# Kernel optimization log

Hardware: AMD Instinct MI355X
Metric: run time of the kernel (lower is better)

Reference implementation:

```python
import jax, jax.numpy as jnp
import numpy as np

N_NODES = 64
N_EDGES = N_NODES * (N_NODES - 1)  # 4032 (fully connected, no self-loops)
BATCH = 64
N_IN = 64
N_HID = 128
N_OUT = 16


def _linear_params(key, fan_in, fan_out):
    # mimic torch nn.Linear default init: U(-1/sqrt(fan_in), 1/sqrt(fan_in))
    kw, kb = jax.random.split(key)
    s = 1.0 / np.sqrt(fan_in)
    W = jax.random.uniform(kw, (fan_in, fan_out), minval=-s, maxval=s, dtype=jnp.float32)
    b = jax.random.uniform(kb, (fan_out,), minval=-s, maxval=s, dtype=jnp.float32)
    return W, b


def setup_inputs() -> dict:
    key = jax.random.key(0)
    ks = jax.random.split(key, 10)
    # one-hot relation matrices for fully-connected graph without self loops
    pairs = np.array([(i, j) for i in range(N_NODES) for j in range(N_NODES) if i != j])
    eye = np.eye(N_NODES, dtype=np.float32)
    rel_send = jnp.asarray(eye[pairs[:, 0]])  # [E, N]
    rel_rec = jnp.asarray(eye[pairs[:, 1]])   # [E, N]

    x = jax.random.normal(ks[0], (BATCH, N_NODES, N_IN), dtype=jnp.float32)

    w1a, b1a = _linear_params(ks[1], N_IN, N_HID)
    w1b, b1b = _linear_params(ks[2], N_HID, N_HID)
    w2a, b2a = _linear_params(ks[3], 2 * N_HID, N_HID)
    w2b, b2b = _linear_params(ks[4], N_HID, N_HID)
    w3a, b3a = _linear_params(ks[5], N_HID, N_HID)
    w3b, b3b = _linear_params(ks[6], N_HID, N_HID)
    w4a, b4a = _linear_params(ks[7], 3 * N_HID, N_HID)  # factor=True
    w4b, b4b = _linear_params(ks[8], N_HID, N_HID)
    wout, bout = _linear_params(ks[9], N_HID, N_OUT)

    return dict(x=x, rel_rec=rel_rec, rel_send=rel_send,
                w1a=w1a, b1a=b1a, w1b=w1b, b1b=b1b,
                w2a=w2a, b2a=b2a, w2b=w2b, b2b=b2b,
                w3a=w3a, b3a=b3a, w3b=w3b, b3b=b3b,
                w4a=w4a, b4a=b4a, w4b=w4b, b4b=b4b,
                wout=wout, bout=bout)


def _mlp(x, wa, ba, wb, bb):
    # Linear -> ReLU -> Linear
    return jax.nn.relu(x @ wa + ba) @ wb + bb


def reference(x, rel_rec, rel_send,
              w1a, b1a, w1b, b1b,
              w2a, b2a, w2b, b2b,
              w3a, b3a, w3b, b3b,
              w4a, b4a, w4b, b4b,
              wout, bout):
    def node2edge(h):
        receivers = jnp.einsum('en,bnh->beh', rel_rec, h)
        senders = jnp.einsum('en,bnh->beh', rel_send, h)
        return jnp.concatenate([senders, receivers], axis=-1)  # [B,E,2H]

    def edge2node(e):
        agg = jnp.einsum('en,beh->bnh', rel_rec, e)
        norm = rel_rec.sum(0)[None, :, None]  # [1,N,1]
        return agg / (norm + 1e-6)

    h = _mlp(x, w1a, b1a, w1b, b1b)            # [B,N,H]
    e = _mlp(node2edge(h), w2a, b2a, w2b, b2b)  # [B,E,H]
    x_skip = e
    # factor=True branch
    n = _mlp(edge2node(e), w3a, b3a, w3b, b3b)  # [B,N,H]
    e2 = node2edge(n)                           # [B,E,2H]
    e2 = jnp.concatenate([e2, x_skip], axis=2)  # [B,E,3H]
    e2 = _mlp(e2, w4a, b4a, w4b, b4b)           # [B,E,H]
    return e2 @ wout + bout                     # [B,E,n_out]
```

## Files before the change

### kernel.cpp

```cpp
#include <hip/hip_runtime.h>
#include <hip/hip_bf16.h>


#define DI __device__ __forceinline__

typedef short bf16x8 __attribute__((ext_vector_type(8)));
typedef float f32x4 __attribute__((ext_vector_type(4)));
typedef unsigned short u16;

static constexpr int NN = 64, NE = 4032, H = 128;

DI u16 f2bf(float f) {
  union { float f; unsigned u; } v; v.f = f;
  unsigned u = v.u;
  return (u16)((u + 0x7fffu + ((u >> 16) & 1u)) >> 16);
}
DI unsigned pk2(float a, float b) {
  union { __hip_bfloat162 h; unsigned u; } c;
  c.h = __float22bfloat162_rn(float2{a, b});
  return c.u;
}
DI f32x4 mf(bf16x8 a, bf16x8 b, f32x4 c) {
  return __builtin_amdgcn_mfma_f32_16x16x32_bf16(a, b, c, 0, 0, 0);
}
DI bf16x8 ldfrag(const u16* __restrict__ p, int idx, int l) {
  return *reinterpret_cast<const bf16x8*>(p + (idx * 64 + l) * 8);
}
#define PIN_REGS() asm volatile("" ::: "memory")

__global__ __launch_bounds__(64) void prepack_kernel(
    const float* __restrict__ w1a, const float* __restrict__ w1b,
    const float* __restrict__ w2a, const float* __restrict__ w2b,
    const float* __restrict__ w3a, const float* __restrict__ w3b,
    const float* __restrict__ w4a, const float* __restrict__ w4b,
    const float* __restrict__ wout,
    const float* __restrict__ b2b, const float* __restrict__ b4b,
    const float* __restrict__ bout,
    u16* __restrict__ pk, float* __restrict__ c2, float* __restrict__ c4) {
  int seg = blockIdx.y, f = blockIdx.x, l = threadIdx.x;
  int h = l >> 4, mm = l & 15;
  if (seg == 10) {
    if (f >= 4) return;
    union { u16 u[8]; uint4 q; } o;
#pragma unroll
    for (int jj = 0; jj < 8; jj++) {
      int row = f * 32 + (jj >> 2) * 16 + h * 4 + (jj & 3);
      float s = 0.f;
      for (int j = 0; j < 128; j++) s += w4b[row * 128 + j] * wout[j * 16 + mm];
      o.u[jj] = f2bf(s);
    }
    *reinterpret_cast<uint4*>(pk + ((304 + f) * 64 + l) * 8) = o.q;
    return;
  }
  if (seg == 11) {
    if (f < 2) {
      int o = f * 64 + l;
      float s = 0.f;
      for (int k = 0; k < 128; k++) s += b2b[k] * w4a[(256 + k) * 128 + o];
      c2[o] = s;
    } else if (f == 2 && l < 16) {
      float s = bout[l];
      for (int k = 0; k < 128; k++) s += b4b[k] * wout[k * 16 + l];
      c4[l] = s;
    }
    return;
  }
  const float* src; int foff, nfrag, roff, pi;
  switch (seg) {
    case 0:  src = w1a; foff = 0;   nfrag = 16; roff = 0;   pi = 0; break;
    case 1:  src = w1b; foff = 16;  nfrag = 32; roff = 0;   pi = 1; break;
    case 2:  src = w2a; foff = 48;  nfrag = 32; roff = 0;   pi = 1; break;
    case 3:  src = w2a; foff = 80;  nfrag = 32; roff = 128; pi = 1; break;
    case 4:  src = w2b; foff = 112; nfrag = 32; roff = 0;   pi = 0; break;
    case 5:  src = w3a; foff = 144; nfrag = 32; roff = 0;   pi = 1; break;
    case 6:  src = w3b; foff = 176; nfrag = 32; roff = 0;   pi = 1; break;
    case 7:  src = w4a; foff = 208; nfrag = 32; roff = 0;   pi = 1; break;
    case 8:  src = w4a; foff = 240; nfrag = 32; roff = 128; pi = 1; break;
    default: src = w4a; foff = 272; nfrag = 32; roff = 256; pi = 1; break;
  }
  if (f >= nfrag) return;
  int kt = f >> 3, ct = f & 7;
  union { u16 u[8]; uint4 q; } o;
#pragma unroll
  for (int jj = 0; jj < 8; jj++) {
    int row = pi ? (kt * 32 + (jj >> 2) * 16 + h * 4 + (jj & 3))
                 : (kt * 32 + h * 8 + jj);
    o.u[jj] = f2bf(src[(roff + row) * 128 + ct * 16 + mm]);
  }
  *reinterpret_cast<uint4*>(pk + ((foff + f) * 64 + l) * 8) = o.q;
}

__global__ __launch_bounds__(64, 1) void node_kernel(
    const float* __restrict__ x, const u16* __restrict__ pk,
    const float* __restrict__ b1a, const float* __restrict__ b1b,
    const float* __restrict__ b2a,
    float* __restrict__ sproj, float* __restrict__ rproj) {
  int blk = blockIdx.x, b = blk >> 2, nq = blk & 3;
  int l = threadIdx.x, m = l & 15, h = l >> 4;
  int node = nq * 16 + m;
  const f32x4 Z = {0.f, 0.f, 0.f, 0.f};
  bf16x8 wA[32], wB[32];
#pragma unroll
  for (int i = 0; i < 16; i++) wA[i] = ldfrag(pk, i, l);
#pragma unroll
  for (int i = 0; i < 32; i++) wB[i] = ldfrag(pk + 16 * 512, i, l);
  PIN_REGS();
  f32x4 acc[8]; bf16x8 ef[4];
  const float* xb = x + (b * NN + node) * 64;
#pragma unroll
  for (int kt = 0; kt < 2; kt++) {
    f32x4 a0 = *(const f32x4*)(xb + kt * 32 + h * 8);
    f32x4 a1 = *(const f32x4*)(xb + kt * 32 + h * 8 + 4);
    union { unsigned u[4]; bf16x8 v; } t;
    t.u[0] = pk2(a0[0], a0[1]); t.u[1] = pk2(a0[2], a0[3]);
    t.u[2] = pk2(a1[0], a1[1]); t.u[3] = pk2(a1[2], a1[3]);
#pragma unroll
    for (int ft = 0; ft < 8; ft++)
      acc[ft] = mf(wA[kt * 8 + ft], t.v, kt == 0 ? Z : acc[ft]);
  }
#pragma unroll
  for (int k2 = 0; k2 < 4; k2++) {
    f32x4 bA = *(const f32x4*)(b1a + (2 * k2) * 16 + h * 4);
    f32x4 bB = *(const f32x4*)(b1a + (2 * k2 + 1) * 16 + h * 4);
    f32x4 a0 = acc[2 * k2], a1 = acc[2 * k2 + 1];
    union { unsigned u[4]; bf16x8 v; } t;
    t.u[0] = pk2(fmaxf(a0[0] + bA[0], 0.f), fmaxf(a0[1] + bA[1], 0.f));
    t.u[1] = pk2(fmaxf(a0[2] + bA[2], 0.f), fmaxf(a0[3] + bA[3], 0.f));
    t.u[2] = pk2(fmaxf(a1[0] + bB[0], 0.f), fmaxf(a1[1] + bB[1], 0.f));
    t.u[3] = pk2(fmaxf(a1[2] + bB[2], 0.f), fmaxf(a1[3] + bB[3], 0.f));
    ef[k2] = t.v;
  }
#pragma unroll
  for (int i = 0; i < 32; i++) wA[i] = ldfrag(pk + 48 * 512, i, l);
  PIN_REGS();
#pragma unroll
  for (int kt = 0; kt < 4; kt++)
#pragma unroll
    for (int ft = 0; ft < 8; ft++)
      acc[ft] = mf(wB[kt * 8 + ft], ef[kt], kt == 0 ? Z : acc[ft]);
  bf16x8 efh[4];
#pragma unroll
  for (int k2 = 0; k2 < 4; k2++) {
    f32x4 bA = *(const f32x4*)(b1b + (2 * k2) * 16 + h * 4);
    f32x4 bB = *(const f32x4*)(b1b + (2 * k2 + 1) * 16 + h * 4);
    f32x4 a0 = acc[2 * k2], a1 = acc[2 * k2 + 1];
    union { unsigned u[4]; bf16x8 v; } t;
    t.u[0] = pk2(a0[0] + bA[0], a0[1] + bA[1]);
    t.u[1] = pk2(a0[2] + bA[2], a0[3] + bA[3]);
    t.u[2] = pk2(a1[0] + bB[0], a1[1] + bB[1]);
    t.u[3] = pk2(a1[2] + bB[2], a1[3] + bB[3]);
    efh[k2] = t.v;
  }
#pragma unroll
  for (int i = 0; i < 32; i++) wB[i] = ldfrag(pk + 80 * 512, i, l);
  PIN_REGS();
#pragma unroll
  for (int kt = 0; kt < 4; kt++)
#pragma unroll
    for (int ft = 0; ft < 8; ft++)
      acc[ft] = mf(wA[kt * 8 + ft], efh[kt], kt == 0 ? Z : acc[ft]);
  float* spo = sproj + (b * NN + node) * H;
#pragma unroll
  for (int ft = 0; ft < 8; ft++)
    *reinterpret_cast<f32x4*>(spo + ft * 16 + h * 4) = acc[ft];
#pragma unroll
  for (int kt = 0; kt < 4; kt++)
#pragma unroll
    for (int ft = 0; ft < 8; ft++)
      acc[ft] = mf(wB[kt * 8 + ft], efh[kt], kt == 0 ? Z : acc[ft]);
  float* rpo = rproj + (b * NN + node) * H;
#pragma unroll
  for (int ft = 0; ft < 8; ft++) {
    f32x4 bb = *(const f32x4*)(b2a + ft * 16 + h * 4);
    f32x4 o = acc[ft];
    o[0] += bb[0]; o[1] += bb[1]; o[2] += bb[2]; o[3] += bb[3];
    *reinterpret_cast<f32x4*>(rpo + ft * 16 + h * 4) = o;
  }
}

__global__ __launch_bounds__(256, 1) void agg_kernel(
    const float* __restrict__ sproj, const float* __restrict__ rproj,
    const u16* __restrict__ pk,
    const float* __restrict__ b2b, const float* __restrict__ b3a,
    const float* __restrict__ b3b, const float* __restrict__ b4a,
    const float* __restrict__ c2,
    float* __restrict__ s4, float* __restrict__ r4) {
  __shared__ float lred[3][32][65];
  int blk = blockIdx.x, b = blk >> 2, jq = blk & 3;
  int tid = threadIdx.x, l = tid & 63, w = tid >> 6, m = l & 15, h = l >> 4;
  int j = jq * 16 + m;
  const float* rpb = rproj + (b * NN + j) * H;
  f32x4 rpv[8], accS[8];
#pragma unroll
  for (int k = 0; k < 8; k++) {
    rpv[k] = *(const f32x4*)(rpb + (k >> 1) * 32 + h * 8 + (k & 1) * 4);
    accS[k] = f32x4{0.f, 0.f, 0.f, 0.f};
  }
  const float* spb = sproj + b * NN * H;
  for (int i = w * 16; i < w * 16 + 16; i++) {
    const float* sp = spb + i * H;
#pragma unroll
    for (int k = 0; k < 8; k++) {
      f32x4 s = *(const f32x4*)(sp + (k >> 1) * 32 + h * 8 + (k & 1) * 4);
      f32x4 t = s + rpv[k];
      t[0] = fmaxf(t[0], 0.f); t[1] = fmaxf(t[1], 0.f);
      t[2] = fmaxf(t[2], 0.f); t[3] = fmaxf(t[3], 0.f);
      accS[k] += t;
    }
  }
  if (w == jq) {
    const float* sp = spb + j * H;
#pragma unroll
    for (int k = 0; k < 8; k++) {
      f32x4 s = *(const f32x4*)(sp + (k >> 1) * 32 + h * 8 + (k & 1) * 4);
      f32x4 t = s + rpv[k];
      accS[k][0] -= fmaxf(t[0], 0.f); accS[k][1] -= fmaxf(t[1], 0.f);
      accS[k][2] -= fmaxf(t[2], 0.f); accS[k][3] -= fmaxf(t[3], 0.f);
    }
  }
  if (w > 0) {
#pragma unroll
    for (int k = 0; k < 8; k++)
#pragma unroll
      for (int qq = 0; qq < 4; qq++) lred[w - 1][k * 4 + qq][l] = accS[k][qq];
  }
  __syncthreads();
  if (w != 0) return;
#pragma unroll
  for (int ww = 0; ww < 3; ww++)
#pragma unroll
    for (int k = 0; k < 8; k++)
#pragma unroll
      for (int qq = 0; qq < 4; qq++) accS[k][qq] += lred[ww][k * 4 + qq][l];

  const f32x4 Z = {0.f, 0.f, 0.f, 0.f};
  bf16x8 tb[4];
#pragma unroll
  for (int k2 = 0; k2 < 4; k2++) {
    f32x4 a0 = accS[2 * k2], a1 = accS[2 * k2 + 1];
    union { unsigned u[4]; bf16x8 v; } t;
    t.u[0] = pk2(a0[0], a0[1]); t.u[1] = pk2(a0[2], a0[3]);
    t.u[2] = pk2(a1[0], a1[1]); t.u[3] = pk2(a1[2], a1[3]);
    tb[k2] = t.v;
  }
  bf16x8 wA[32], wB[32]; f32x4 acc[8]; bf16x8 ef[4], efn[4];
#pragma unroll
  for (int i = 0; i < 32; i++) wA[i] = ldfrag(pk + 112 * 512, i, l);
#pragma unroll
  for (int i = 0; i < 32; i++) wB[i] = ldfrag(pk + 144 * 512, i, l);
  PIN_REGS();
#pragma unroll
  for (int kt = 0; kt < 4; kt++)
#pragma unroll
    for (int ft = 0; ft < 8; ft++)
      acc[ft] = mf(wA[kt * 8 + ft], tb[kt], kt == 0 ? Z : acc[ft]);
  const float inv = 1.0f / (63.0f + 1e-6f);
  const float binv = 63.0f * inv;
#pragma unroll
  for (int k2 = 0; k2 < 4; k2++) {
    f32x4 bA = *(const f32x4*)(b2b + (2 * k2) * 16 + h * 4);
    f32x4 bB = *(const f32x4*)(b2b + (2 * k2 + 1) * 16 + h * 4);
    f32x4 a0 = acc[2 * k2], a1 = acc[2 * k2 + 1];
    union { unsigned u[4]; bf16x8 v; } t;
    t.u[0] = pk2(a0[0] * inv + bA[0] * binv, a0[1] * inv + bA[1] * binv);
    t.u[1] = pk2(a0[2] * inv + bA[2] * binv, a0[3] * inv + bA[3] * binv);
    t.u[2] = pk2(a1[0] * inv + bB[0] * binv, a1[1] * inv + bB[1] * binv);
    t.u[3] = pk2(a1[2] * inv + bB[2] * binv, a1[3] * inv + bB[3] * binv);
    ef[k2] = t.v;
  }
#pragma unroll
  for (int i = 0; i < 32; i++) wA[i] = ldfrag(pk + 176 * 512, i, l);
  PIN_REGS();
#pragma unroll
  for (int kt = 0; kt < 4; kt++)
#pragma unroll
    for (int ft = 0; ft < 8; ft++)
      acc[ft] = mf(wB[kt * 8 + ft], ef[kt], kt == 0 ? Z : acc[ft]);
#pragma unroll
  for (int k2 = 0; k2 < 4; k2++) {
    f32x4 bA = *(const f32x4*)(b3a + (2 * k2) * 16 + h * 4);
    f32x4 bB = *(const f32x4*)(b3a + (2 * k2 + 1) * 16 + h * 4);
    f32x4 a0 = acc[2 * k2], a1 = acc[2 * k2 + 1];
    union { unsigned u[4]; bf16x8 v; } t;
    t.u[0] = pk2(fmaxf(a0[0] + bA[0], 0.f), fmaxf(a0[1] + bA[1], 0.f));
    t.u[1] = pk2(fmaxf(a0[2] + bA[2], 0.f), fmaxf(a0[3] + bA[3], 0.f));
    t.u[2] = pk2(fmaxf(a1[0] + bB[0], 0.f), fmaxf(a1[1] + bB[1], 0.f));
    t.u[3] = pk2(fmaxf(a1[2] + bB[2], 0.f), fmaxf(a1[3] + bB[3], 0.f));
    ef[k2] = t.v;
  }
#pragma unroll
  for (int i = 0; i < 32; i++) wB[i] = ldfrag(pk + 208 * 512, i, l);
  PIN_REGS();
#pragma unroll
  for (int kt = 0; kt < 4; kt++)
#pragma unroll
    for (int ft = 0; ft < 8; ft++)
      acc[ft] = mf(wA[kt * 8 + ft], ef[kt], kt == 0 ? Z : acc[ft]);
#pragma unroll
  for (int k2 = 0; k2 < 4; k2++) {
    f32x4 bA = *(const f32x4*)(b3b + (2 * k2) * 16 + h * 4);
    f32x4 bB = *(const f32x4*)(b3b + (2 * k2 + 1) * 16 + h * 4);
    f32x4 a0 = acc[2 * k2], a1 = acc[2 * k2 + 1];
    union { unsigned u[4]; bf16x8 v; } t;
    t.u[0] = pk2(a0[0] + bA[0], a0[1] + bA[1]);
    t.u[1] = pk2(a0[2] + bA[2], a0[3] + bA[3]);
    t.u[2] = pk2(a1[0] + bB[0], a1[1] + bB[1]);
    t.u[3] = pk2(a1[2] + bB[2], a1[3] + bB[3]);
    efn[k2] = t.v;
  }
#pragma unroll
  for (int i = 0; i < 32; i++) wA[i] = ldfrag(pk + 240 * 512, i, l);
  PIN_REGS();
#pragma unroll
  for (int kt = 0; kt < 4; kt++)
#pragma unroll
    for (int ft = 0; ft < 8; ft++)
      acc[ft] = mf(wB[kt * 8 + ft], efn[kt], kt == 0 ? Z : acc[ft]);
  float* s4o = s4 + (b * NN + j) * H;
#pragma unroll
  for (int ft = 0; ft < 8; ft++) {
    f32x4 cc = *(const f32x4*)(c2 + ft * 16 + h * 4);
    f32x4 o = acc[ft];
    o[0] += cc[0]; o[1] += cc[1]; o[2] += cc[2]; o[3] += cc[3];
    *reinterpret_cast<f32x4*>(s4o + ft * 16 + h * 4) = o;
  }
#pragma unroll
  for (int kt = 0; kt < 4; kt++)
#pragma unroll
    for (int ft = 0; ft < 8; ft++)
      acc[ft] = mf(wA[kt * 8 + ft], efn[kt], kt == 0 ? Z : acc[ft]);
  float* r4o = r4 + (b * NN + j) * H;
#pragma unroll
  for (int ft = 0; ft < 8; ft++) {
    f32x4 bb = *(const f32x4*)(b4a + ft * 16 + h * 4);
    f32x4 o = acc[ft];
    o[0] += bb[0]; o[1] += bb[1]; o[2] += bb[2]; o[3] += bb[3];
    *reinterpret_cast<f32x4*>(r4o + ft * 16 + h * 4) = o;
  }
}

__global__ __launch_bounds__(256, 2) void edge_kernel(
    const float* __restrict__ sproj, const float* __restrict__ rproj,
    const float* __restrict__ s4, const float* __restrict__ r4,
    const u16* __restrict__ pk, const float* __restrict__ c4,
    float* __restrict__ out) {
  __shared__ alignas(16) u16 w2l[32 * 512];
  __shared__ alignas(16) u16 w4l[32 * 512];
  int blk = blockIdx.x;
  int b = blk >> 4, ig = blk & 15;
  int tid = threadIdx.x, l = tid & 63, w = tid >> 6;
  int m = l & 15, h = l >> 4;
#pragma unroll
  for (int it = 0; it < 8; it++) {
    int idx = it * 256 + tid;
    *reinterpret_cast<uint4*>(&w2l[idx * 8]) =
        *reinterpret_cast<const uint4*>(pk + 112 * 512 + idx * 8);
    *reinterpret_cast<uint4*>(&w4l[idx * 8]) =
        *reinterpret_cast<const uint4*>(pk + 272 * 512 + idx * 8);
  }
  bf16x8 wfv[4];
#pragma unroll
  for (int i2 = 0; i2 < 4; i2++) wfv[i2] = ldfrag(pk + 304 * 512, i2, l);
  f32x4 c4v = *(const f32x4*)(c4 + h * 4);
  int i = ig * 4 + w;
  const float* sp  = sproj + (b * NN + i) * H;
  const float* s4p = s4 + (b * NN + i) * H;
  const float* rpb = rproj + b * NN * H;
  const float* r4b = r4 + b * NN * H;
  const float* rp[4];
  const float* r4p[4];
#pragma unroll
  for (int mt = 0; mt < 4; mt++) {
    int jj = mt * 16 + m;
    int v = jj + (jj >= i ? 1 : 0); v = v > 63 ? 63 : v;
    rp[mt] = rpb + v * H;
    r4p[mt] = r4b + v * H;
  }
  __syncthreads();
  const f32x4 Z = {0.f, 0.f, 0.f, 0.f};
  f32x4 acc[4][8];
  bf16x8 ef[4][4];
#pragma unroll
  for (int kt = 0; kt < 4; kt++) {
    f32x4 s0 = *(const f32x4*)(sp + kt * 32 + h * 8);
    f32x4 s1 = *(const f32x4*)(sp + kt * 32 + h * 8 + 4);
    bf16x8 tb[4];
#pragma unroll
    for (int mt = 0; mt < 4; mt++) {
      f32x4 r0 = *(const f32x4*)(rp[mt] + kt * 32 + h * 8);
      f32x4 r1 = *(const f32x4*)(rp[mt] + kt * 32 + h * 8 + 4);
      union { unsigned u[4]; bf16x8 v; } t;
      t.u[0] = pk2(fmaxf(r0[0] + s0[0], 0.f), fmaxf(r0[1] + s0[1], 0.f));
      t.u[1] = pk2(fmaxf(r0[2] + s0[2], 0.f), fmaxf(r0[3] + s0[3], 0.f));
      t.u[2] = pk2(fmaxf(r1[0] + s1[0], 0.f), fmaxf(r1[1] + s1[1], 0.f));
      t.u[3] = pk2(fmaxf(r1[2] + s1[2], 0.f), fmaxf(r1[3] + s1[3], 0.f));
      tb[mt] = t.v;
    }
#pragma unroll
    for (int ft = 0; ft < 8; ft++) {
      bf16x8 wv = *reinterpret_cast<const bf16x8*>(&w2l[((kt * 8 + ft) * 64 + l) * 8]);
#pragma unroll
      for (int mt = 0; mt < 4; mt++)
        acc[mt][ft] = mf(wv, tb[mt], kt == 0 ? Z : acc[mt][ft]);
    }
  }
#pragma unroll
  for (int mt = 0; mt < 4; mt++)
#pragma unroll
    for (int k2 = 0; k2 < 4; k2++) {
      f32x4 a0 = acc[mt][2 * k2], a1 = acc[mt][2 * k2 + 1];
      union { unsigned u[4]; bf16x8 v; } t2;
      t2.u[0] = pk2(a0[0], a0[1]); t2.u[1] = pk2(a0[2], a0[3]);
      t2.u[2] = pk2(a1[0], a1[1]); t2.u[3] = pk2(a1[2], a1[3]);
      ef[mt][k2] = t2.v;
    }
#pragma unroll
  for (int kt = 0; kt < 4; kt++)
#pragma unroll
    for (int ft = 0; ft < 8; ft++) {
      bf16x8 wv = *reinterpret_cast<const bf16x8*>(&w4l[((kt * 8 + ft) * 64 + l) * 8]);
#pragma unroll
      for (int mt = 0; mt < 4; mt++)
        acc[mt][ft] = mf(wv, ef[mt][kt], kt == 0 ? Z : acc[mt][ft]);
    }
#pragma unroll
  for (int k2 = 0; k2 < 4; k2++) {
    f32x4 sA = *(const f32x4*)(s4p + (2 * k2) * 16 + h * 4);
    f32x4 sB = *(const f32x4*)(s4p + (2 * k2 + 1) * 16 + h * 4);
#pragma unroll
    for (int mt = 0; mt < 4; mt++) {
      f32x4 rA = *(const f32x4*)(r4p[mt] + (2 * k2) * 16 + h * 4);
      f32x4 rB = *(const f32x4*)(r4p[mt] + (2 * k2 + 1) * 16 + h * 4);
      f32x4 a0 = acc[mt][2 * k2], a1 = acc[mt][2 * k2 + 1];
      union { unsigned u[4]; bf16x8 v; } t2;
      t2.u[0] = pk2(fmaxf(a0[0] + sA[0] + rA[0], 0.f), fmaxf(a0[1] + sA[1] + rA[1], 0.f));
      t2.u[1] = pk2(fmaxf(a0[2] + sA[2] + rA[2], 0.f), fmaxf(a0[3] + sA[3] + rA[3], 0.f));
      t2.u[2] = pk2(fmaxf(a1[0] + sB[0] + rB[0], 0.f), fmaxf(a1[1] + sB[1] + rB[1], 0.f));
      t2.u[3] = pk2(fmaxf(a1[2] + sB[2] + rB[2], 0.f), fmaxf(a1[3] + sB[3] + rB[3], 0.f));
      ef[mt][k2] = t2.v;
    }
  }
#pragma unroll
  for (int mt = 0; mt < 4; mt++) {
    f32x4 a4 = Z;
#pragma unroll
    for (int kt = 0; kt < 4; kt++) a4 = mf(wfv[kt], ef[mt][kt], a4);
    int jj = mt * 16 + m;
    if (jj < 63) {
      f32x4 o;
      o[0] = a4[0] + c4v[0]; o[1] = a4[1] + c4v[1];
      o[2] = a4[2] + c4v[2]; o[3] = a4[3] + c4v[3];
      *reinterpret_cast<f32x4*>(out + (b * NE + i * 63 + jj) * 16 + h * 4) = o;
    }
  }
}

extern "C" void kernel_launch(void* const* d_in, const int* in_sizes, int n_in,
                              void* d_out, int out_size, void* d_ws, size_t ws_size,
                              hipStream_t stream) {
  const float* x    = (const float*)d_in[0];
  const float* w1a  = (const float*)d_in[3];
  const float* b1a  = (const float*)d_in[4];
  const float* w1b  = (const float*)d_in[5];
  const float* b1b  = (const float*)d_in[6];
  const float* w2a  = (const float*)d_in[7];
  const float* b2a  = (const float*)d_in[8];
  const float* w2b  = (const float*)d_in[9];
  const float* b2b  = (const float*)d_in[10];
  const float* w3a  = (const float*)d_in[11];
  const float* b3a  = (const float*)d_in[12];
  const float* w3b  = (const float*)d_in[13];
  const float* b3b  = (const float*)d_in[14];
  const float* w4a  = (const float*)d_in[15];
  const float* b4a  = (const float*)d_in[16];
  const float* w4b  = (const float*)d_in[17];
  const float* b4b  = (const float*)d_in[18];
  const float* wout = (const float*)d_in[19];
  const float* bout = (const float*)d_in[20];
  float* out = (float*)d_out;

  float* sproj = (float*)d_ws;
  float* rproj = sproj + 524288;
  float* s4    = rproj + 524288;
  float* r4    = s4 + 524288;
  u16* pkw     = (u16*)(r4 + 524288);
  float* c2    = (float*)(pkw + 174080);
  float* c4    = c2 + 128;

  prepack_kernel<<<dim3(32, 12), 64, 0, stream>>>(
      w1a, w1b, w2a, w2b, w3a, w3b, w4a, w4b, wout, b2b, b4b, bout, pkw, c2, c4);
  node_kernel<<<256, 64, 0, stream>>>(x, pkw, b1a, b1b, b2a, sproj, rproj);
  agg_kernel<<<256, 256, 0, stream>>>(sproj, rproj, pkw, b2b, b3a, b3b, b4a, c2, s4, r4);
  edge_kernel<<<1024, 256, 0, stream>>>(sproj, rproj, s4, r4, pkw, c4, out);
}
```

Baseline: 101.4 us.

## Split node/agg MLPs across four waves and halve edge tile per wave

The node kernel now uses 256 threads, and the MLP tail of the agg kernel now runs on all four waves instead of one. Each wave computes two of the eight output column tiles, and activations are exchanged through shared memory with barriers between layers. The edge kernel gives each wave half of a sender row and reuses a single shared weight buffer for both layers, which cuts LDS use and allows three blocks per CU and twice as many blocks. The aim is to remove serial single-wave MLP chains and raise occupancy, at the cost of extra barriers, repeated global weight-fragment loads, and a weight reload in the edge kernel.

Result: no change. 101.2 us (-0.2%).

```diff
diff --git a/kernel.cpp b/kernel.cpp
--- a/kernel.cpp
+++ b/kernel.cpp
@@ -26,7 +26,6 @@
 DI bf16x8 ldfrag(const u16* __restrict__ p, int idx, int l) {
   return *reinterpret_cast<const bf16x8*>(p + (idx * 64 + l) * 8);
 }
-#define PIN_REGS() asm volatile("" ::: "memory")
 
 __global__ __launch_bounds__(64) void prepack_kernel(
     const float* __restrict__ w1a, const float* __restrict__ w1b,
@@ -90,102 +89,100 @@
   *reinterpret_cast<uint4*>(pk + ((foff + f) * 64 + l) * 8) = o.q;
 }
 
-__global__ __launch_bounds__(64, 1) void node_kernel(
+__global__ __launch_bounds__(256, 4) void node_kernel(
     const float* __restrict__ x, const u16* __restrict__ pk,
     const float* __restrict__ b1a, const float* __restrict__ b1b,
     const float* __restrict__ b2a,
     float* __restrict__ sproj, float* __restrict__ rproj) {
+  __shared__ bf16x8 act[2][4][64];
   int blk = blockIdx.x, b = blk >> 2, nq = blk & 3;
-  int l = threadIdx.x, m = l & 15, h = l >> 4;
+  int tid = threadIdx.x, l = tid & 63, w = tid >> 6;
+  int m = l & 15, h = l >> 4;
   int node = nq * 16 + m;
   const f32x4 Z = {0.f, 0.f, 0.f, 0.f};
-  bf16x8 wA[32], wB[32];
-#pragma unroll
-  for (int i = 0; i < 16; i++) wA[i] = ldfrag(pk, i, l);
-#pragma unroll
-  for (int i = 0; i < 32; i++) wB[i] = ldfrag(pk + 16 * 512, i, l);
-  PIN_REGS();
-  f32x4 acc[8]; bf16x8 ef[4];
-  const float* xb = x + (b * NN + node) * 64;
-#pragma unroll
-  for (int kt = 0; kt < 2; kt++) {
-    f32x4 a0 = *(const f32x4*)(xb + kt * 32 + h * 8);
-    f32x4 a1 = *(const f32x4*)(xb + kt * 32 + h * 8 + 4);
-    union { unsigned u[4]; bf16x8 v; } t;
-    t.u[0] = pk2(a0[0], a0[1]); t.u[1] = pk2(a0[2], a0[3]);
-    t.u[2] = pk2(a1[0], a1[1]); t.u[3] = pk2(a1[2], a1[3]);
-#pragma unroll
-    for (int ft = 0; ft < 8; ft++)
-      acc[ft] = mf(wA[kt * 8 + ft], t.v, kt == 0 ? Z : acc[ft]);
-  }
-#pragma unroll
-  for (int k2 = 0; k2 < 4; k2++) {
-    f32x4 bA = *(const f32x4*)(b1a + (2 * k2) * 16 + h * 4);
-    f32x4 bB = *(const f32x4*)(b1a + (2 * k2 + 1) * 16 + h * 4);
-    f32x4 a0 = acc[2 * k2], a1 = acc[2 * k2 + 1];
-    union { unsigned u[4]; bf16x8 v; } t;
-    t.u[0] = pk2(fmaxf(a0[0] + bA[0], 0.f), fmaxf(a0[1] + bA[1], 0.f));
-    t.u[1] = pk2(fmaxf(a0[2] + bA[2], 0.f), fmaxf(a0[3] + bA[3], 0.f));
-    t.u[2] = pk2(fmaxf(a1[0] + bB[0], 0.f), fmaxf(a1[1] + bB[1], 0.f));
-    t.u[3] = pk2(fmaxf(a1[2] + bB[2], 0.f), fmaxf(a1[3] + bB[3], 0.f));
-    ef[k2] = t.v;
-  }
-#pragma unroll
-  for (int i = 0; i < 32; i++) wA[i] = ldfrag(pk + 48 * 512, i, l);
-  PIN_REGS();
-#pragma unroll
-  for (int kt = 0; kt < 4; kt++)
-#pragma unroll
-    for (int ft = 0; ft < 8; ft++)
-      acc[ft] = mf(wB[kt * 8 + ft], ef[kt], kt == 0 ? Z : acc[ft]);
-  bf16x8 efh[4];
-#pragma unroll
-  for (int k2 = 0; k2 < 4; k2++) {
-    f32x4 bA = *(const f32x4*)(b1b + (2 * k2) * 16 + h * 4);
-    f32x4 bB = *(const f32x4*)(b1b + (2 * k2 + 1) * 16 + h * 4);
-    f32x4 a0 = acc[2 * k2], a1 = acc[2 * k2 + 1];
-    union { unsigned u[4]; bf16x8 v; } t;
-    t.u[0] = pk2(a0[0] + bA[0], a0[1] + bA[1]);
-    t.u[1] = pk2(a0[2] + bA[2], a0[3] + bA[3]);
-    t.u[2] = pk2(a1[0] + bB[0], a1[1] + bB[1]);
-    t.u[3] = pk2(a1[2] + bB[2], a1[3] + bB[3]);
-    efh[k2] = t.v;
-  }
-#pragma unroll
-  for (int i = 0; i < 32; i++) wB[i] = ldfrag(pk + 80 * 512, i, l);
-  PIN_REGS();
-#pragma unroll
-  for (int kt = 0; kt < 4; kt++)
-#pragma unroll
-    for (int ft = 0; ft < 8; ft++)
-      acc[ft] = mf(wA[kt * 8 + ft], efh[kt], kt == 0 ? Z : acc[ft]);
+  f32x4 acc0, acc1;
+  {
+    const float* xb = x + (b * NN + node) * 64;
+    bf16x8 xin[2];
+#pragma unroll
+    for (int kt = 0; kt < 2; kt++) {
+      f32x4 a0 = *(const f32x4*)(xb + kt * 32 + h * 8);
+      f32x4 a1 = *(const f32x4*)(xb + kt * 32 + h * 8 + 4);
+      union { unsigned u[4]; bf16x8 v; } t;
+      t.u[0] = pk2(a0[0], a0[1]); t.u[1] = pk2(a0[2], a0[3]);
+      t.u[2] = pk2(a1[0], a1[1]); t.u[3] = pk2(a1[2], a1[3]);
+      xin[kt] = t.v;
+    }
+#pragma unroll
+    for (int kt = 0; kt < 2; kt++) {
+      acc0 = mf(ldfrag(pk, kt * 8 + 2 * w, l),     xin[kt], kt == 0 ? Z : acc0);
+      acc1 = mf(ldfrag(pk, kt * 8 + 2 * w + 1, l), xin[kt], kt == 0 ? Z : acc1);
+    }
+    f32x4 bA = *(const f32x4*)(b1a + (2 * w) * 16 + h * 4);
+    f32x4 bB = *(const f32x4*)(b1a + (2 * w + 1) * 16 + h * 4);
+    union { unsigned u[4]; bf16x8 v; } t;
+    t.u[0] = pk2(fmaxf(acc0[0] + bA[0], 0.f), fmaxf(acc0[1] + bA[1], 0.f));
+    t.u[1] = pk2(fmaxf(acc0[2] + bA[2], 0.f), fmaxf(acc0[3] + bA[3], 0.f));
+    t.u[2] = pk2(fmaxf(acc1[0] + bB[0], 0.f), fmaxf(acc1[1] + bB[1], 0.f));
+    t.u[3] = pk2(fmaxf(acc1[2] + bB[2], 0.f), fmaxf(acc1[3] + bB[3], 0.f));
+    act[0][w][l] = t.v;
+  }
+  __syncthreads();
+  bf16x8 ef[4];
+#pragma unroll
+  for (int kt = 0; kt < 4; kt++) ef[kt] = act[0][kt][l];
+#pragma unroll
+  for (int kt = 0; kt < 4; kt++) {
+    acc0 = mf(ldfrag(pk + 16 * 512, kt * 8 + 2 * w, l),     ef[kt], kt == 0 ? Z : acc0);
+    acc1 = mf(ldfrag(pk + 16 * 512, kt * 8 + 2 * w + 1, l), ef[kt], kt == 0 ? Z : acc1);
+  }
+  {
+    f32x4 bA = *(const f32x4*)(b1b + (2 * w) * 16 + h * 4);
+    f32x4 bB = *(const f32x4*)(b1b + (2 * w + 1) * 16 + h * 4);
+    union { unsigned u[4]; bf16x8 v; } t;
+    t.u[0] = pk2(acc0[0] + bA[0], acc0[1] + bA[1]);
+    t.u[1] = pk2(acc0[2] + bA[2], acc0[3] + bA[3]);
+    t.u[2] = pk2(acc1[0] + bB[0], acc1[1] + bB[1]);
+    t.u[3] = pk2(acc1[2] + bB[2], acc1[3] + bB[3]);
+    act[1][w][l] = t.v;
+  }
+  __syncthreads();
+#pragma unroll
+  for (int kt = 0; kt < 4; kt++) ef[kt] = act[1][kt][l];
+#pragma unroll
+  for (int kt = 0; kt < 4; kt++) {
+    acc0 = mf(ldfrag(pk + 48 * 512, kt * 8 + 2 * w, l),     ef[kt], kt == 0 ? Z : acc0);
+    acc1 = mf(ldfrag(pk + 48 * 512, kt * 8 + 2 * w + 1, l), ef[kt], kt == 0 ? Z : acc1);
+  }
   float* spo = sproj + (b * NN + node) * H;
-#pragma unroll
-  for (int ft = 0; ft < 8; ft++)
-    *reinterpret_cast<f32x4*>(spo + ft * 16 + h * 4) = acc[ft];
-#pragma unroll
-  for (int kt = 0; kt < 4; kt++)
-#pragma unroll
-    for (int ft = 0; ft < 8; ft++)
-      acc[ft] = mf(wB[kt * 8 + ft], efh[kt], kt == 0 ? Z : acc[ft]);
-  float* rpo = rproj + (b * NN + node) * H;
-#pragma unroll
-  for (int ft = 0; ft < 8; ft++) {
-    f32x4 bb = *(const f32x4*)(b2a + ft * 16 + h * 4);
-    f32x4 o = acc[ft];
-    o[0] += bb[0]; o[1] += bb[1]; o[2] += bb[2]; o[3] += bb[3];
-    *reinterpret_cast<f32x4*>(rpo + ft * 16 + h * 4) = o;
-  }
-}
-
-__global__ __launch_bounds__(256, 1) void agg_kernel(
+  *reinterpret_cast<f32x4*>(spo + (2 * w) * 16 + h * 4) = acc0;
+  *reinterpret_cast<f32x4*>(spo + (2 * w + 1) * 16 + h * 4) = acc1;
+#pragma unroll
+  for (int kt = 0; kt < 4; kt++) {
+    acc0 = mf(ldfrag(pk + 80 * 512, kt * 8 + 2 * w, l),     ef[kt], kt == 0 ? Z : acc0);
+    acc1 = mf(ldfrag(pk + 80 * 512, kt * 8 + 2 * w + 1, l), ef[kt], kt == 0 ? Z : acc1);
+  }
+  {
+    f32x4 bA = *(const f32x4*)(b2a + (2 * w) * 16 + h * 4);
+    f32x4 bB = *(const f32x4*)(b2a + (2 * w + 1) * 16 + h * 4);
+    float* rpo = rproj + (b * NN + node) * H;
+    f32x4 o0 = acc0, o1 = acc1;
+    o0[0] += bA[0]; o0[1] += bA[1]; o0[2] += bA[2]; o0[3] += bA[3];
+    o1[0] += bB[0]; o1[1] += bB[1]; o1[2] += bB[2]; o1[3] += bB[3];
+    *reinterpret_cast<f32x4*>(rpo + (2 * w) * 16 + h * 4) = o0;
+    *reinterpret_cast<f32x4*>(rpo + (2 * w + 1) * 16 + h * 4) = o1;
+  }
+}
+
+__global__ __launch_bounds__(256, 3) void agg_kernel(
     const float* __restrict__ sproj, const float* __restrict__ rproj,
     const u16* __restrict__ pk,
     const float* __restrict__ b2b, const float* __restrict__ b3a,
     const float* __restrict__ b3b, const float* __restrict__ b4a,
     const float* __restrict__ c2,
     float* __restrict__ s4, float* __restrict__ r4) {
-  __shared__ float lred[3][32][65];
+  __shared__ f32x4 lred[4][8][64];
+  __shared__ bf16x8 act[2][4][64];
   int blk = blockIdx.x, b = blk >> 2, jq = blk & 3;
   int tid = threadIdx.x, l = tid & 63, w = tid >> 6, m = l & 15, h = l >> 4;
   int j = jq * 16 + m;
@@ -218,177 +215,151 @@
       accS[k][2] -= fmaxf(t[2], 0.f); accS[k][3] -= fmaxf(t[3], 0.f);
     }
   }
-  if (w > 0) {
-#pragma unroll
-    for (int k = 0; k < 8; k++)
-#pragma unroll
-      for (int qq = 0; qq < 4; qq++) lred[w - 1][k * 4 + qq][l] = accS[k][qq];
-  }
-  __syncthreads();
-  if (w != 0) return;
-#pragma unroll
-  for (int ww = 0; ww < 3; ww++)
-#pragma unroll
-    for (int k = 0; k < 8; k++)
-#pragma unroll
-      for (int qq = 0; qq < 4; qq++) accS[k][qq] += lred[ww][k * 4 + qq][l];
-
+#pragma unroll
+  for (int k = 0; k < 8; k++) lred[w][k][l] = accS[k];
+  __syncthreads();
+  {
+    f32x4 s0 = lred[0][2 * w][l] + lred[1][2 * w][l] + lred[2][2 * w][l] + lred[3][2 * w][l];
+    f32x4 s1 = lred[0][2 * w + 1][l] + lred[1][2 * w + 1][l] + lred[2][2 * w + 1][l] + lred[3][2 * w + 1][l];
+    union { unsigned u[4]; bf16x8 v; } t;
+    t.u[0] = pk2(s0[0], s0[1]); t.u[1] = pk2(s0[2], s0[3]);
+    t.u[2] = pk2(s1[0], s1[1]); t.u[3] = pk2(s1[2], s1[3]);
+    act[0][w][l] = t.v;
+  }
+  __syncthreads();
   const f32x4 Z = {0.f, 0.f, 0.f, 0.f};
-  bf16x8 tb[4];
-#pragma unroll
-  for (int k2 = 0; k2 < 4; k2++) {
-    f32x4 a0 = accS[2 * k2], a1 = accS[2 * k2 + 1];
-    union { unsigned u[4]; bf16x8 v; } t;
-    t.u[0] = pk2(a0[0], a0[1]); t.u[1] = pk2(a0[2], a0[3]);
-    t.u[2] = pk2(a1[0], a1[1]); t.u[3] = pk2(a1[2], a1[3]);
-    tb[k2] = t.v;
-  }
-  bf16x8 wA[32], wB[32]; f32x4 acc[8]; bf16x8 ef[4], efn[4];
-#pragma unroll
-  for (int i = 0; i < 32; i++) wA[i] = ldfrag(pk + 112 * 512, i, l);
-#pragma unroll
-  for (int i = 0; i < 32; i++) wB[i] = ldfrag(pk + 144 * 512, i, l);
-  PIN_REGS();
-#pragma unroll
-  for (int kt = 0; kt < 4; kt++)
-#pragma unroll
-    for (int ft = 0; ft < 8; ft++)
-      acc[ft] = mf(wA[kt * 8 + ft], tb[kt], kt == 0 ? Z : acc[ft]);
-  const float inv = 1.0f / (63.0f + 1e-6f);
-  const float binv = 63.0f * inv;
-#pragma unroll
-  for (int k2 = 0; k2 < 4; k2++) {
-    f32x4 bA = *(const f32x4*)(b2b + (2 * k2) * 16 + h * 4);
-    f32x4 bB = *(const f32x4*)(b2b + (2 * k2 + 1) * 16 + h * 4);
-    f32x4 a0 = acc[2 * k2], a1 = acc[2 * k2 + 1];
-    union { unsigned u[4]; bf16x8 v; } t;
-    t.u[0] = pk2(a0[0] * inv + bA[0] * binv, a0[1] * inv + bA[1] * binv);
-    t.u[1] = pk2(a0[2] * inv + bA[2] * binv, a0[3] * inv + bA[3] * binv);
-    t.u[2] = pk2(a1[0] * inv + bB[0] * binv, a1[1] * inv + bB[1] * binv);
-    t.u[3] = pk2(a1[2] * inv + bB[2] * binv, a1[3] * inv + bB[3] * binv);
-    ef[k2] = t.v;
-  }
-#pragma unroll
-  for (int i = 0; i < 32; i++) wA[i] = ldfrag(pk + 176 * 512, i, l);
-  PIN_REGS();
-#pragma unroll
-  for (int kt = 0; kt < 4; kt++)
-#pragma unroll
-    for (int ft = 0; ft < 8; ft++)
-      acc[ft] = mf(wB[kt * 8 + ft], ef[kt], kt == 0 ? Z : acc[ft]);
-#pragma unroll
-  for (int k2 = 0; k2 < 4; k2++) {
-    f32x4 bA = *(const f32x4*)(b3a + (2 * k2) * 16 + h * 4);
-    f32x4 bB = *(const f32x4*)(b3a + (2 * k2 + 1) * 16 + h * 4);
-    f32x4 a0 = acc[2 * k2], a1 = acc[2 * k2 + 1];
-    union { unsigned u[4]; bf16x8 v; } t;
-    t.u[0] = pk2(fmaxf(a0[0] + bA[0], 0.f), fmaxf(a0[1] + bA[1], 0.f));
-    t.u[1] = pk2(fmaxf(a0[2] + bA[2], 0.f), fmaxf(a0[3] + bA[3], 0.f));
-    t.u[2] = pk2(fmaxf(a1[0] + bB[0], 0.f), fmaxf(a1[1] + bB[1], 0.f));
-    t.u[3] = pk2(fmaxf(a1[2] + bB[2], 0.f), fmaxf(a1[3] + bB[3], 0.f));
-    ef[k2] = t.v;
-  }
-#pragma unroll
-  for (int i = 0; i < 32; i++) wB[i] = ldfrag(pk + 208 * 512, i, l);
-  PIN_REGS();
-#pragma unroll
-  for (int kt = 0; kt < 4; kt++)
-#pragma unroll
-    for (int ft = 0; ft < 8; ft++)
-      acc[ft] = mf(wA[kt * 8 + ft], ef[kt], kt == 0 ? Z : acc[ft]);
-#pragma unroll
-  for (int k2 = 0; k2 < 4; k2++) {
-    f32x4 bA = *(const f32x4*)(b3b + (2 * k2) * 16 + h * 4);
-    f32x4 bB = *(const f32x4*)(b3b + (2 * k2 + 1) * 16 + h * 4);
-    f32x4 a0 = acc[2 * k2], a1 = acc[2 * k2 + 1];
-    union { unsigned u[4]; bf16x8 v; } t;
-    t.u[0] = pk2(a0[0] + bA[0], a0[1] + bA[1]);
-    t.u[1] = pk2(a0[2] + bA[2], a0[3] + bA[3]);
-    t.u[2] = pk2(a1[0] + bB[0], a1[1] + bB[1]);
-    t.u[3] = pk2(a1[2] + bB[2], a1[3] + bB[3]);
-    efn[k2] = t.v;
-  }
-#pragma unroll
-  for (int i = 0; i < 32; i++) wA[i] = ldfrag(pk + 240 * 512, i, l);
-  PIN_REGS();
-#pragma unroll
-  for (int kt = 0; kt < 4; kt++)
-#pragma unroll
-    for (int ft = 0; ft < 8; ft++)
-      acc[ft] = mf(wB[kt * 8 + ft], efn[kt], kt == 0 ? Z : acc[ft]);
-  float* s4o = s4 + (b * NN + j) * H;
-#pragma unroll
-  for (int ft = 0; ft < 8; ft++) {
-    f32x4 cc = *(const f32x4*)(c2 + ft * 16 + h * 4);
-    f32x4 o = acc[ft];
-    o[0] += cc[0]; o[1] += cc[1]; o[2] += cc[2]; o[3] += cc[3];
-    *reinterpret_cast<f32x4*>(s4o + ft * 16 + h * 4) = o;
-  }
-#pragma unroll
-  for (int kt = 0; kt < 4; kt++)
-#pragma unroll
-    for (int ft = 0; ft < 8; ft++)
-      acc[ft] = mf(wA[kt * 8 + ft], efn[kt], kt == 0 ? Z : acc[ft]);
-  float* r4o = r4 + (b * NN + j) * H;
-#pragma unroll
-  for (int ft = 0; ft < 8; ft++) {
-    f32x4 bb = *(const f32x4*)(b4a + ft * 16 + h * 4);
-    f32x4 o = acc[ft];
-    o[0] += bb[0]; o[1] += bb[1]; o[2] += bb[2]; o[3] += bb[3];
-    *reinterpret_cast<f32x4*>(r4o + ft * 16 + h * 4) = o;
-  }
-}
-
-__global__ __launch_bounds__(256, 2) void edge_kernel(
+  f32x4 acc0, acc1;
+  bf16x8 ef[4];
+#pragma unroll
+  for (int kt = 0; kt < 4; kt++) ef[kt] = act[0][kt][l];
+#pragma unroll
+  for (int kt = 0; kt < 4; kt++) {
+    acc0 = mf(ldfrag(pk + 112 * 512, kt * 8 + 2 * w, l),     ef[kt], kt == 0 ? Z : acc0);
+    acc1 = mf(ldfrag(pk + 112 * 512, kt * 8 + 2 * w + 1, l), ef[kt], kt == 0 ? Z : acc1);
+  }
+  {
+    const float inv = 1.0f / (63.0f + 1e-6f);
+    const float binv = 63.0f * inv;
+    f32x4 bA = *(const f32x4*)(b2b + (2 * w) * 16 + h * 4);
+    f32x4 bB = *(const f32x4*)(b2b + (2 * w + 1) * 16 + h * 4);
+    union { unsigned u[4]; bf16x8 v; } t;
+    t.u[0] = pk2(acc0[0] * inv + bA[0] * binv, acc0[1] * inv + bA[1] * binv);
+    t.u[1] = pk2(acc0[2] * inv + bA[2] * binv, acc0[3] * inv + bA[3] * binv);
+    t.u[2] = pk2(acc1[0] * inv + bB[0] * binv, acc1[1] * inv + bB[1] * binv);
+    t.u[3] = pk2(acc1[2] * inv + bB[2] * binv, acc1[3] * inv + bB[3] * binv);
+    act[1][w][l] = t.v;
+  }
+  __syncthreads();
+#pragma unroll
+  for (int kt = 0; kt < 4; kt++) ef[kt] = act[1][kt][l];
+#pragma unroll
+  for (int kt = 0; kt < 4; kt++) {
+    acc0 = mf(ldfrag(pk + 144 * 512, kt * 8 + 2 * w, l),     ef[kt], kt == 0 ? Z : acc0);
+    acc1 = mf(ldfrag(pk + 144 * 512, kt * 8 + 2 * w + 1, l), ef[kt], kt == 0 ? Z : acc1);
+  }
+  {
+    f32x4 bA = *(const f32x4*)(b3a + (2 * w) * 16 + h * 4);
+    f32x4 bB = *(const f32x4*)(b3a + (2 * w + 1) * 16 + h * 4);
+    union { unsigned u[4]; bf16x8 v; } t;
+    t.u[0] = pk2(fmaxf(acc0[0] + bA[0], 0.f), fmaxf(acc0[1] + bA[1], 0.f));
+    t.u[1] = pk2(fmaxf(acc0[2] + bA[2], 0.f), fmaxf(acc0[3] + bA[3], 0.f));
+    t.u[2] = pk2(fmaxf(acc1[0] + bB[0], 0.f), fmaxf(acc1[1] + bB[1], 0.f));
+    t.u[3] = pk2(fmaxf(acc1[2] + bB[2], 0.f), fmaxf(acc1[3] + bB[3], 0.f));
+    act[0][w][l] = t.v;
+  }
+  __syncthreads();
+#pragma unroll
+  for (int kt = 0; kt < 4; kt++) ef[kt] = act[0][kt][l];
+#pragma unroll
+  for (int kt = 0; kt < 4; kt++) {
+    acc0 = mf(ldfrag(pk + 176 * 512, kt * 8 + 2 * w, l),     ef[kt], kt == 0 ? Z : acc0);
+    acc1 = mf(ldfrag(pk + 176 * 512, kt * 8 + 2 * w + 1, l), ef[kt], kt == 0 ? Z : acc1);
+  }
+  {
+    f32x4 bA = *(const f32x4*)(b3b + (2 * w) * 16 + h * 4);
+    f32x4 bB = *(const f32x4*)(b3b + (2 * w + 1) * 16 + h * 4);
+    union { unsigned u[4]; bf16x8 v; } t;
+    t.u[0] = pk2(acc0[0] + bA[0], acc0[1] + bA[1]);
+    t.u[1] = pk2(acc0[2] + bA[2], acc0[3] + bA[3]);
+    t.u[2] = pk2(acc1[0] + bB[0], acc1[1] + bB[1]);
+    t.u[3] = pk2(acc1[2] + bB[2], acc1[3] + bB[3]);
+    act[1][w][l] = t.v;
+  }
+  __syncthreads();
+#pragma unroll
+  for (int kt = 0; kt < 4; kt++) ef[kt] = act[1][kt][l];
+#pragma unroll
+  for (int kt = 0; kt < 4; kt++) {
+    acc0 = mf(ldfrag(pk + 208 * 512, kt * 8 + 2 * w, l),     ef[kt], kt == 0 ? Z : acc0);
+    acc1 = mf(ldfrag(pk + 208 * 512, kt * 8 + 2 * w + 1, l), ef[kt], kt == 0 ? Z : acc1);
+  }
+  {
+    f32x4 cA = *(const f32x4*)(c2 + (2 * w) * 16 + h * 4);
+    f32x4 cB = *(const f32x4*)(c2 + (2 * w + 1) * 16 + h * 4);
+    float* s4o = s4 + (b * NN + j) * H;
+    f32x4 o0 = acc0, o1 = acc1;
+    o0[0] += cA[0]; o0[1] += cA[1]; o0[2] += cA[2]; o0[3] += cA[3];
+    o1[0] += cB[0]; o1[1] += cB[1]; o1[2] += cB[2]; o1[3] += cB[3];
+    *reinterpret_cast<f32x4*>(s4o + (2 * w) * 16 + h * 4) = o0;
+    *reinterpret_cast<f32x4*>(s4o + (2 * w + 1) * 16 + h * 4) = o1;
+  }
+#pragma unroll
+  for (int kt = 0; kt < 4; kt++) {
+    acc0 = mf(ldfrag(pk + 240 * 512, kt * 8 + 2 * w, l),     ef[kt], kt == 0 ? Z : acc0);
+    acc1 = mf(ldfrag(pk + 240 * 512, kt * 8 + 2 * w + 1, l), ef[kt], kt == 0 ? Z : acc1);
+  }
+  {
+    f32x4 bA = *(const f32x4*)(b4a + (2 * w) * 16 + h * 4);
+    f32x4 bB = *(const f32x4*)(b4a + (2 * w + 1) * 16 + h * 4);
+    float* r4o = r4 + (b * NN + j) * H;
+    f32x4 o0 = acc0, o1 = acc1;
+    o0[0] += bA[0]; o0[1] += bA[1]; o0[2] += bA[2]; o0[3] += bA[3];
+    o1[0] += bB[0]; o1[1] += bB[1]; o1[2] += bB[2]; o1[3] += bB[3];
+    *reinterpret_cast<f32x4*>(r4o + (2 * w) * 16 + h * 4) = o0;
+    *reinterpret_cast<f32x4*>(r4o + (2 * w + 1) * 16 + h * 4) = o1;
+  }
+}
+
+__global__ __launch_bounds__(256, 3) void edge_kernel(
     const float* __restrict__ sproj, const float* __restrict__ rproj,
     const float* __restrict__ s4, const float* __restrict__ r4,
     const u16* __restrict__ pk, const float* __restrict__ c4,
     float* __restrict__ out) {
-  __shared__ alignas(16) u16 w2l[32 * 512];
-  __shared__ alignas(16) u16 w4l[32 * 512];
+  __shared__ alignas(16) u16 wl[32 * 512];
   int blk = blockIdx.x;
-  int b = blk >> 4, ig = blk & 15;
+  int b = blk >> 5, sg = blk & 31;
   int tid = threadIdx.x, l = tid & 63, w = tid >> 6;
   int m = l & 15, h = l >> 4;
+  int i = sg * 2 + (w >> 1);
+  int hf = w & 1;
 #pragma unroll
   for (int it = 0; it < 8; it++) {
     int idx = it * 256 + tid;
-    *reinterpret_cast<uint4*>(&w2l[idx * 8]) =
+    *reinterpret_cast<uint4*>(&wl[idx * 8]) =
         *reinterpret_cast<const uint4*>(pk + 112 * 512 + idx * 8);
-    *reinterpret_cast<uint4*>(&w4l[idx * 8]) =
-        *reinterpret_cast<const uint4*>(pk + 272 * 512 + idx * 8);
-  }
-  bf16x8 wfv[4];
-#pragma unroll
-  for (int i2 = 0; i2 < 4; i2++) wfv[i2] = ldfrag(pk + 304 * 512, i2, l);
-  f32x4 c4v = *(const f32x4*)(c4 + h * 4);
-  int i = ig * 4 + w;
+  }
   const float* sp  = sproj + (b * NN + i) * H;
-  const float* s4p = s4 + (b * NN + i) * H;
   const float* rpb = rproj + b * NN * H;
-  const float* r4b = r4 + b * NN * H;
-  const float* rp[4];
-  const float* r4p[4];
-#pragma unroll
-  for (int mt = 0; mt < 4; mt++) {
-    int jj = mt * 16 + m;
-    int v = jj + (jj >= i ? 1 : 0); v = v > 63 ? 63 : v;
-    rp[mt] = rpb + v * H;
-    r4p[mt] = r4b + v * H;
+  int jn[2];
+#pragma unroll
+  for (int mt = 0; mt < 2; mt++) {
+    int jj = (hf * 2 + mt) * 16 + m;
+    int v = jj + (jj >= i ? 1 : 0); jn[mt] = v > 63 ? 63 : v;
   }
   __syncthreads();
   const f32x4 Z = {0.f, 0.f, 0.f, 0.f};
-  f32x4 acc[4][8];
-  bf16x8 ef[4][4];
+  f32x4 acc[2][8];
+  bf16x8 ef[2][4];
 #pragma unroll
   for (int kt = 0; kt < 4; kt++) {
     f32x4 s0 = *(const f32x4*)(sp + kt * 32 + h * 8);
     f32x4 s1 = *(const f32x4*)(sp + kt * 32 + h * 8 + 4);
-    bf16x8 tb[4];
-#pragma unroll
-    for (int mt = 0; mt < 4; mt++) {
-      f32x4 r0 = *(const f32x4*)(rp[mt] + kt * 32 + h * 8);
-      f32x4 r1 = *(const f32x4*)(rp[mt] + kt * 32 + h * 8 + 4);
+    bf16x8 tb[2];
+#pragma unroll
+    for (int mt = 0; mt < 2; mt++) {
+      const float* rp = rpb + jn[mt] * H;
+      f32x4 r0 = *(const f32x4*)(rp + kt * 32 + h * 8);
+      f32x4 r1 = *(const f32x4*)(rp + kt * 32 + h * 8 + 4);
       union { unsigned u[4]; bf16x8 v; } t;
       t.u[0] = pk2(fmaxf(r0[0] + s0[0], 0.f), fmaxf(r0[1] + s0[1], 0.f));
       t.u[1] = pk2(fmaxf(r0[2] + s0[2], 0.f), fmaxf(r0[3] + s0[3], 0.f));
@@ -398,14 +369,14 @@
     }
 #pragma unroll
     for (int ft = 0; ft < 8; ft++) {
-      bf16x8 wv = *reinterpret_cast<const bf16x8*>(&w2l[((kt * 8 + ft) * 64 + l) * 8]);
-#pragma unroll
-      for (int mt = 0; mt < 4; mt++)
+      bf16x8 wv = *reinterpret_cast<const bf16x8*>(&wl[((kt * 8 + ft) * 64 + l) * 8]);
+#pragma unroll
+      for (int mt = 0; mt < 2; mt++)
         acc[mt][ft] = mf(wv, tb[mt], kt == 0 ? Z : acc[mt][ft]);
     }
   }
 #pragma unroll
-  for (int mt = 0; mt < 4; mt++)
+  for (int mt = 0; mt < 2; mt++)
 #pragma unroll
     for (int k2 = 0; k2 < 4; k2++) {
       f32x4 a0 = acc[mt][2 * k2], a1 = acc[mt][2 * k2 + 1];
@@ -414,43 +385,62 @@
       t2.u[2] = pk2(a1[0], a1[1]); t2.u[3] = pk2(a1[2], a1[3]);
       ef[mt][k2] = t2.v;
     }
+  __syncthreads();
+#pragma unroll
+  for (int it = 0; it < 8; it++) {
+    int idx = it * 256 + tid;
+    *reinterpret_cast<uint4*>(&wl[idx * 8]) =
+        *reinterpret_cast<const uint4*>(pk + 272 * 512 + idx * 8);
+  }
+  __syncthreads();
 #pragma unroll
   for (int kt = 0; kt < 4; kt++)
 #pragma unroll
     for (int ft = 0; ft < 8; ft++) {
-      bf16x8 wv = *reinterpret_cast<const bf16x8*>(&w4l[((kt * 8 + ft) * 64 + l) * 8]);
-#pragma unroll
-      for (int mt = 0; mt < 4; mt++)
+      bf16x8 wv = *reinterpret_cast<const bf16x8*>(&wl[((kt * 8 + ft) * 64 + l) * 8]);
+#pragma unroll
+      for (int mt = 0; mt < 2; mt++)
         acc[mt][ft] = mf(wv, ef[mt][kt], kt == 0 ? Z : acc[mt][ft]);
     }
-#pragma unroll
-  for (int k2 = 0; k2 < 4; k2++) {
-    f32x4 sA = *(const f32x4*)(s4p + (2 * k2) * 16 + h * 4);
-    f32x4 sB = *(const f32x4*)(s4p + (2 * k2 + 1) * 16 + h * 4);
-#pragma unroll
-    for (int mt = 0; mt < 4; mt++) {
-      f32x4 rA = *(const f32x4*)(r4p[mt] + (2 * k2) * 16 + h * 4);
-      f32x4 rB = *(const f32x4*)(r4p[mt] + (2 * k2 + 1) * 16 + h * 4);
-      f32x4 a0 = acc[mt][2 * k2], a1 = acc[mt][2 * k2 + 1];
-      union { unsigned u[4]; bf16x8 v; } t2;
-      t2.u[0] = pk2(fmaxf(a0[0] + sA[0] + rA[0], 0.f), fmaxf(a0[1] + sA[1] + rA[1], 0.f));
-      t2.u[1] = pk2(fmaxf(a0[2] + sA[2] + rA[2], 0.f), fmaxf(a0[3] + sA[3] + rA[3], 0.f));
-      t2.u[2] = pk2(fmaxf(a1[0] + sB[0] + rB[0], 0.f), fmaxf(a1[1] + sB[1] + rB[1], 0.f));
-      t2.u[3] = pk2(fmaxf(a1[2] + sB[2] + rB[2], 0.f), fmaxf(a1[3] + sB[3] + rB[3], 0.f));
-      ef[mt][k2] = t2.v;
-    }
-  }
-#pragma unroll
-  for (int mt = 0; mt < 4; mt++) {
-    f32x4 a4 = Z;
-#pragma unroll
-    for (int kt = 0; kt < 4; kt++) a4 = mf(wfv[kt], ef[mt][kt], a4);
-    int jj = mt * 16 + m;
-    if (jj < 63) {
-      f32x4 o;
-      o[0] = a4[0] + c4v[0]; o[1] = a4[1] + c4v[1];
-      o[2] = a4[2] + c4v[2]; o[3] = a4[3] + c4v[3];
-      *reinterpret_cast<f32x4*>(out + (b * NE + i * 63 + jj) * 16 + h * 4) = o;
+  {
+    const float* s4p = s4 + (b * NN + i) * H;
+    const float* r4b = r4 + b * NN * H;
+#pragma unroll
+    for (int k2 = 0; k2 < 4; k2++) {
+      f32x4 sA = *(const f32x4*)(s4p + (2 * k2) * 16 + h * 4);
+      f32x4 sB = *(const f32x4*)(s4p + (2 * k2 + 1) * 16 + h * 4);
+#pragma unroll
+      for (int mt = 0; mt < 2; mt++) {
+        const float* r4p = r4b + jn[mt] * H;
+        f32x4 rA = *(const f32x4*)(r4p + (2 * k2) * 16 + h * 4);
+        f32x4 rB = *(const f32x4*)(r4p + (2 * k2 + 1) * 16 + h * 4);
+        f32x4 a0 = acc[mt][2 * k2], a1 = acc[mt][2 * k2 + 1];
+        union { unsigned u[4]; bf16x8 v; } t2;
+        t2.u[0] = pk2(fmaxf(a0[0] + sA[0] + rA[0], 0.f), fmaxf(a0[1] + sA[1] + rA[1], 0.f));
+        t2.u[1] = pk2(fmaxf(a0[2] + sA[2] + rA[2], 0.f), fmaxf(a0[3] + sA[3] + rA[3], 0.f));
+        t2.u[2] = pk2(fmaxf(a1[0] + sB[0] + rB[0], 0.f), fmaxf(a1[1] + sB[1] + rB[1], 0.f));
+        t2.u[3] = pk2(fmaxf(a1[2] + sB[2] + rB[2], 0.f), fmaxf(a1[3] + sB[3] + rB[3], 0.f));
+        ef[mt][k2] = t2.v;
+      }
+    }
+  }
+  {
+    bf16x8 wfv[4];
+#pragma unroll
+    for (int i2 = 0; i2 < 4; i2++) wfv[i2] = ldfrag(pk + 304 * 512, i2, l);
+    f32x4 c4v = *(const f32x4*)(c4 + h * 4);
+#pragma unroll
+    for (int mt = 0; mt < 2; mt++) {
+      f32x4 a4 = Z;
+#pragma unroll
+      for (int kt = 0; kt < 4; kt++) a4 = mf(wfv[kt], ef[mt][kt], a4);
+      int jj = (hf * 2 + mt) * 16 + m;
+      if (jj < 63) {
+        f32x4 o;
+        o[0] = a4[0] + c4v[0]; o[1] = a4[1] + c4v[1];
+        o[2] = a4[2] + c4v[2]; o[3] = a4[3] + c4v[3];
+        *reinterpret_cast<f32x4*>(out + (b * NE + i * 63 + jj) * 16 + h * 4) = o;
+      }
     }
   }
 }
@@ -489,7 +479,7 @@
 
   prepack_kernel<<<dim3(32, 12), 64, 0, stream>>>(
       w1a, w1b, w2a, w2b, w3a, w3b, w4a, w4b, wout, b2b, b4b, bout, pkw, c2, c4);
-  node_kernel<<<256, 64, 0, stream>>>(x, pkw, b1a, b1b, b2a, sproj, rproj);
+  node_kernel<<<256, 256, 0, stream>>>(x, pkw, b1a, b1b, b2a, sproj, rproj);
   agg_kernel<<<256, 256, 0, stream>>>(sproj, rproj, pkw, b2b, b3a, b3b, b4a, c2, s4, r4);
-  edge_kernel<<<1024, 256, 0, stream>>>(sproj, rproj, s4, r4, pkw, c4, out);
-}
+  edge_kernel<<<2048, 256, 0, stream>>>(sproj, rproj, s4, r4, pkw, c4, out);
+}
```
